# Kernel tuning notes

Measured on AMD Instinct MI355X. Metric: run time of the kernel, lower is better.

Reference implementation:

```python
import jax, jax.numpy as jnp
import numpy as np

IN_DIM = 256
MEM_DIM = 256
DEPTH = 18                    # complete binary tree
N = 2 ** DEPTH - 1            # 262143 nodes; children of i are 2i+1, 2i+2; node 0 is root


def _glorot(k, shape):
    lim = float(np.sqrt(6.0 / (shape[0] + shape[1])))
    return jax.random.uniform(k, shape, jnp.float32, -lim, lim)


def setup_inputs() -> dict:
    key = jax.random.key(0)
    ks = jax.random.split(key, 6)
    inputs = jax.random.normal(ks[0], (N, IN_DIM), jnp.float32)
    Wioux = _glorot(ks[1], (3 * MEM_DIM, IN_DIM))
    bioux = jnp.zeros((3 * MEM_DIM,), jnp.float32)
    Wiouh = _glorot(ks[2], (3 * MEM_DIM, MEM_DIM))
    Wfx = _glorot(ks[3], (MEM_DIM, IN_DIM))
    bfx = jnp.zeros((MEM_DIM,), jnp.float32)
    Wfh = _glorot(ks[4], (MEM_DIM, MEM_DIM))
    fb = jnp.ones((MEM_DIM,), jnp.float32)
    return {"inputs": inputs, "Wioux": Wioux, "bioux": bioux, "Wiouh": Wiouh,
            "Wfx": Wfx, "bfx": bfx, "Wfh": Wfh, "fb": fb}


def reference(inputs, Wioux, bioux, Wiouh, Wfx, bfx, Wfh, fb):
    # Child-Sum TreeLSTM over a complete binary tree, level-wise batched (bottom-up).
    n, _ = inputs.shape
    m = fb.shape[0]
    depth = int(np.log2(n + 1))
    # Input projections for all nodes at once (same math as per-node ioux/fx).
    xiou = inputs @ Wioux.T + bioux          # [N, 3m]
    xf = inputs @ Wfx.T + bfx                # [N, m]
    h_all = jnp.zeros((n, m), inputs.dtype)
    c_all = jnp.zeros((n, m), inputs.dtype)
    for d in range(depth - 1, -1, -1):
        s, e = 2 ** d - 1, 2 ** (d + 1) - 1   # nodes at level d
        if d == depth - 1:
            # Leaves: zero child state -> iouh/fh contribute 0, fc sums to 0.
            i, o, u = jnp.split(xiou[s:e], 3, axis=1)
            i, o, u = jax.nn.sigmoid(i), jax.nn.sigmoid(o), jnp.tanh(u)
            c = i * u
        else:
            node = jnp.arange(s, e)
            ch = jnp.stack([2 * node + 1, 2 * node + 2], axis=1)   # [L, 2]
            ch_h = h_all[ch]                                       # [L, 2, m]
            ch_c = c_all[ch]                                       # [L, 2, m]
            iou = xiou[s:e] + ch_h.sum(axis=1) @ Wiouh.T           # child-sum
            i, o, u = jnp.split(iou, 3, axis=1)
            i, o, u = jax.nn.sigmoid(i), jax.nn.sigmoid(o), jnp.tanh(u)
            f = jax.nn.sigmoid(jnp.einsum('lkm,nm->lkn', ch_h, Wfh)
                               + xf[s:e][:, None, :] + fb)         # per-child forget gate
            c = i * u + (f * ch_c).sum(axis=1)
        h = o * jnp.tanh(c)
        h_all = h_all.at[s:e].set(h)
        c_all = c_all.at[s:e].set(c)
    # (root h, root c, all node hidden states) as in the torch forward
    return h_all[0], c_all[0], h_all
```

## Files before the change

### kernel.cpp

```cpp
#include <hip/hip_runtime.h>


typedef __attribute__((ext_vector_type(8))) short bf16x8;
typedef __attribute__((ext_vector_type(8))) unsigned short us8;
typedef __attribute__((ext_vector_type(4))) float f32x4;
typedef __attribute__((ext_vector_type(4))) float f4;

#define MFMA16(A, B, C) __builtin_amdgcn_mfma_f32_16x16x32_bf16(A, B, C, 0, 0, 0)

__device__ __forceinline__ unsigned short f2b(float f) {
  unsigned int u = __builtin_bit_cast(unsigned int, f);
  u = u + 0x7FFFu + ((u >> 16) & 1u);
  return (unsigned short)(u >> 16);
}
__device__ __forceinline__ float bf2f(unsigned short u) {
  unsigned int v = (unsigned int)u << 16;
  return __builtin_bit_cast(float, v);
}
__device__ __forceinline__ us8 pack8(f4 a, f4 b) {
  us8 r;
  r[0] = f2b(a[0]); r[1] = f2b(a[1]); r[2] = f2b(a[2]); r[3] = f2b(a[3]);
  r[4] = f2b(b[0]); r[5] = f2b(b[1]); r[6] = f2b(b[2]); r[7] = f2b(b[3]);
  return r;
}
__device__ __forceinline__ float sigm(float x) { return 1.0f / (1.0f + __expf(-x)); }
__device__ __forceinline__ float tanh_f(float x) { return 2.0f / (1.0f + __expf(-2.0f * x)) - 1.0f; }

__global__ void pack_w(const float* __restrict__ a,
                       const float* __restrict__ b,
                       const float* __restrict__ c,
                       const float* __restrict__ d,
                       unsigned short* __restrict__ out) {
  int i = blockIdx.x * blockDim.x + threadIdx.x;
  const int A = 768 * 256;
  const int B = A + 768 * 256;
  const int C = B + 256 * 256;
  float v;
  if (i < A)      v = a[i];
  else if (i < B) v = b[i - A];
  else if (i < C) v = c[i - B];
  else            v = d[i - C];
  out[i] = f2b(v);
}

__global__ void conv_x(const float* __restrict__ x, unsigned short* __restrict__ xb, int n8) {
  int i = blockIdx.x * blockDim.x + threadIdx.x;
  if (i >= n8) return;
  f4 a = __builtin_nontemporal_load((const f4*)(x + (size_t)i * 8));
  f4 b = __builtin_nontemporal_load((const f4*)(x + (size_t)i * 8 + 4));
  __builtin_nontemporal_store(pack8(a, b), (us8*)(xb + (size_t)i * 8));
}

template<int LEAF>
__global__ __launch_bounds__(512) __attribute__((amdgpu_waves_per_eu(3, 4)))
void level_k(
    const unsigned short* __restrict__ xb,
    const unsigned short* __restrict__ wb,
    const float* __restrict__ bioux,
    const float* __restrict__ bfx,
    const float* __restrict__ fb,
    float* __restrict__ h_all,
    const unsigned short* __restrict__ hs_r,
    const unsigned short* __restrict__ hbe_r,
    const unsigned int* __restrict__ cp_r,
    unsigned short* __restrict__ hs_w,
    unsigned short* __restrict__ hbe_w,
    unsigned int* __restrict__ cp_w,
    float* __restrict__ out0,
    int s, int L, int T16, int root, int lns)
{
  extern __shared__ unsigned short W[];

  const int tid    = threadIdx.x;
  const int NS     = 1 << lns;
  const int cg     = blockIdx.x >> lns;
  const int stripe = blockIdx.x & (NS - 1);

  const int NP = LEAF ? 3 : 8;
  #pragma unroll 1
  for (int c = tid; c < NP * 512; c += 512) {
    const int p   = c >> 9;
    const int q   = c & 511;
    const int kc  = q >> 6;
    const int kg  = (q >> 4) & 3;
    const int col = q & 15;
    const int po = (p < 3) ? p * 65536
                 : (p < 6) ? 196608 + (p - 3) * 65536
                 : (p == 6) ? 393216 : 458752;
    us8 v = *(const us8*)(wb + po + (size_t)(cg * 16 + col) * 256 + kc * 32 + kg * 8);
    *(us8*)(W + p * 4096 + ((kc * 4 + kg) * 16 + col) * 8) = v;
  }
  __syncthreads();

  const int lane = tid & 63;
  const int wv   = tid >> 6;
  const int lm   = lane & 15;
  const int kgl  = lane >> 4;
  const int colc = cg * 16 + lm;

  const unsigned short* LW = W + kgl * 128 + lm * 8;

  const float bi_ = bioux[colc];
  const float bo_ = bioux[256 + colc];
  const float bu_ = bioux[512 + colc];
  const float bf_ = LEAF ? 0.f : (bfx[colc] + fb[colc]);

  const int Tper = (T16 + NS - 1) >> lns;
  const int t0   = stripe * Tper;
  const int tE   = (t0 + Tper < T16) ? (t0 + Tper) : T16;

  for (int t = t0 + wv; t < tE; t += 8) {
    const int tb16  = t * 16;
    const int drow0 = tb16 + kgl * 4;
    const unsigned short* xr = xb + (size_t)(s + tb16 + lm) * 256 + kgl * 8;
    const f32x4 z4 = {0.f, 0.f, 0.f, 0.f};

    if (!LEAF) {
      const unsigned short* hbr = hbe_r + (size_t)(tb16 + lm) * 256 + kgl * 8;
      const unsigned short* hsr = hs_r  + (size_t)(tb16 + lm) * 256 + kgl * 8;

      unsigned int cpv[4];
      #pragma unroll
      for (int r = 0; r < 4; ++r)
        cpv[r] = cp_r[(size_t)(drow0 + r) * 256 + colc];

      f32x4 xf = z4, f1h = z4, ai = z4, ao = z4, au = z4, fs = z4;
      #pragma unroll 2
      for (int kc = 0; kc < 8; ++kc) {
        bf16x8 ax = *(const bf16x8*)(xr  + kc * 32);
        bf16x8 a1 = *(const bf16x8*)(hbr + kc * 32);
        bf16x8 ah = *(const bf16x8*)(hsr + kc * 32);
        bf16x8 b6 = *(const bf16x8*)(LW + 6 * 4096 + kc * 512);
        bf16x8 b0 = *(const bf16x8*)(LW + 0 * 4096 + kc * 512);
        bf16x8 b1 = *(const bf16x8*)(LW + 1 * 4096 + kc * 512);
        bf16x8 b2 = *(const bf16x8*)(LW + 2 * 4096 + kc * 512);
        bf16x8 b7 = *(const bf16x8*)(LW + 7 * 4096 + kc * 512);
        bf16x8 b3 = *(const bf16x8*)(LW + 3 * 4096 + kc * 512);
        bf16x8 b4 = *(const bf16x8*)(LW + 4 * 4096 + kc * 512);
        bf16x8 b5 = *(const bf16x8*)(LW + 5 * 4096 + kc * 512);
        xf  = MFMA16(ax, b6, xf);
        ai  = MFMA16(ax, b0, ai);
        ao  = MFMA16(ax, b1, ao);
        au  = MFMA16(ax, b2, au);
        f1h = MFMA16(a1, b7, f1h);
        ai  = MFMA16(ah, b3, ai);
        ao  = MFMA16(ah, b4, ao);
        au  = MFMA16(ah, b5, au);
        fs  = MFMA16(ah, b7, fs);
      }

      float hv4[4], cv4[4];
      #pragma unroll
      for (int r = 0; r < 4; ++r) {
        const float i_ = sigm(ai[r] + bi_);
        const float u_ = tanh_f(au[r] + bu_);
        const float o_ = sigm(ao[r] + bo_);
        const float f1 = sigm(xf[r] + f1h[r] + bf_);
        const float f2 = sigm(xf[r] + fs[r] - f1h[r] + bf_);
        const float c1 = bf2f((unsigned short)(cpv[r] & 0xffffu));
        const float c2 = bf2f((unsigned short)(cpv[r] >> 16));
        const float c_ = i_ * u_ + f1 * c1 + f2 * c2;
        const float h_ = o_ * tanh_f(c_);
        cv4[r] = c_; hv4[r] = h_;
        const int j = drow0 + r;
        if (j < L)
          __builtin_nontemporal_store(h_, h_all + (size_t)(s + j) * 256 + colc);
      }
      if (root) {
        if (drow0 == 0) { out0[colc] = hv4[0]; out0[256 + colc] = cv4[0]; }
      } else {
        #pragma unroll
        for (int rp = 0; rp < 2; ++rp) {
          const int j0 = drow0 + rp * 2;
          if (j0 + 1 < L) {
            const int pp = j0 >> 1;
            hs_w [(size_t)pp * 256 + colc] = f2b(hv4[rp*2] + hv4[rp*2+1]);
            hbe_w[(size_t)pp * 256 + colc] = f2b(hv4[rp*2]);
            cp_w [(size_t)pp * 256 + colc] =
                (unsigned int)f2b(cv4[rp*2]) | ((unsigned int)f2b(cv4[rp*2+1]) << 16);
          }
        }
      }
    } else {
      f32x4 ai = z4, ao = z4, au = z4;
      #pragma unroll 4
      for (int kc = 0; kc < 8; ++kc) {
        bf16x8 ax = *(const bf16x8*)(xr + kc * 32);
        bf16x8 b0 = *(const bf16x8*)(LW + 0 * 4096 + kc * 512);
        bf16x8 b1 = *(const bf16x8*)(LW + 1 * 4096 + kc * 512);
        bf16x8 b2 = *(const bf16x8*)(LW + 2 * 4096 + kc * 512);
        ai = MFMA16(ax, b0, ai);
        ao = MFMA16(ax, b1, ao);
        au = MFMA16(ax, b2, au);
      }
      float hv4[4], cv4[4];
      #pragma unroll
      for (int r = 0; r < 4; ++r) {
        const float i_ = sigm(ai[r] + bi_);
        const float u_ = tanh_f(au[r] + bu_);
        const float o_ = sigm(ao[r] + bo_);
        const float c_ = i_ * u_;
        const float h_ = o_ * tanh_f(c_);
        cv4[r] = c_; hv4[r] = h_;
        __builtin_nontemporal_store(h_, h_all + (size_t)(s + drow0 + r) * 256 + colc);
      }
      #pragma unroll
      for (int rp = 0; rp < 2; ++rp) {
        const int pp = (drow0 + rp * 2) >> 1;
        hs_w [(size_t)pp * 256 + colc] = f2b(hv4[rp*2] + hv4[rp*2+1]);
        hbe_w[(size_t)pp * 256 + colc] = f2b(hv4[rp*2]);
        cp_w [(size_t)pp * 256 + colc] =
            (unsigned int)f2b(cv4[rp*2]) | ((unsigned int)f2b(cv4[rp*2+1]) << 16);
      }
    }
  }
}

extern "C" void kernel_launch(void* const* d_in, const int* in_sizes, int n_in,
                              void* d_out, int out_size, void* d_ws, size_t ws_size,
                              hipStream_t stream) {
  const float* inputs = (const float*)d_in[0];
  const float* Wioux  = (const float*)d_in[1];
  const float* bioux  = (const float*)d_in[2];
  const float* Wiouh  = (const float*)d_in[3];
  const float* Wfx    = (const float*)d_in[4];
  const float* bfx    = (const float*)d_in[5];
  const float* Wfh    = (const float*)d_in[6];
  const float* fb     = (const float*)d_in[7];

  const int N = in_sizes[0] / 256;
  int depth = 0;
  while (((1 << depth) - 1) < N) ++depth;

  float* out   = (float*)d_out;
  float* h_all = out + 512;

  static bool attr_done = false;
  if (!attr_done) {
    hipFuncSetAttribute((const void*)level_k<0>,
                        hipFuncAttributeMaxDynamicSharedMemorySize, 8 * 8192);
    hipFuncSetAttribute((const void*)level_k<1>,
                        hipFuncAttributeMaxDynamicSharedMemorySize, 3 * 8192);
    attr_done = true;
  }

  char* p = (char*)d_ws;
  unsigned short* hs0  = (unsigned short*)p; p += (size_t)65536 * 256 * 2;
  unsigned short* hbe0 = (unsigned short*)p; p += (size_t)65536 * 256 * 2;
  unsigned int*   cp0  = (unsigned int*)p;   p += (size_t)65536 * 256 * 4;
  unsigned short* hs1  = (unsigned short*)p; p += (size_t)32768 * 256 * 2;
  unsigned short* hbe1 = (unsigned short*)p; p += (size_t)32768 * 256 * 2;
  unsigned int*   cp1  = (unsigned int*)p;   p += (size_t)32768 * 256 * 4;
  unsigned short* xb   = (unsigned short*)p; p += (size_t)N * 256 * 2;
  unsigned short* wb   = (unsigned short*)p;

  pack_w<<<2048, 256, 0, stream>>>(Wioux, Wiouh, Wfx, Wfh, wb);
  {
    const int n8 = (N * 256) / 8;
    conv_x<<<(n8 + 255) / 256, 256, 0, stream>>>(inputs, xb, n8);
  }

  for (int d = depth - 1; d >= 0; --d) {
    const int L = 1 << d;
    const int s = L - 1;
    const int T16 = (L + 15) / 16;
    int lg = 0; while ((1 << (lg + 1)) <= T16) ++lg;
    int lns = lg - 3; if (lns < 0) lns = 0; if (lns > 5) lns = 5;
    const int rp_ = d & 1, wp_ = (d - 1) & 1;
    const unsigned short* hs_r  = rp_ ? hs1 : hs0;
    const unsigned short* hbe_r = rp_ ? hbe1 : hbe0;
    const unsigned int*   cp_r  = rp_ ? cp1 : cp0;
    unsigned short* hs_w  = wp_ ? hs1 : hs0;
    unsigned short* hbe_w = wp_ ? hbe1 : hbe0;
    unsigned int*   cp_w  = wp_ ? cp1 : cp0;
    if (d == depth - 1) {
      level_k<1><<<16 * 64, 512, 3 * 8192, stream>>>(
          xb, wb, bioux, bfx, fb, h_all,
          hs_r, hbe_r, cp_r, hs_w, hbe_w, cp_w, out, s, L, T16, 0, 6);
    } else {
      level_k<0><<<16 << lns, 512, 8 * 8192, stream>>>(
          xb, wb, bioux, bfx, fb, h_all,
          hs_r, hbe_r, cp_r, hs_w, hbe_w, cp_w, out, s, L, T16, (d == 0) ? 1 : 0, lns);
    }
  }
}
```

Baseline: 803.8 us.

## Store x and child-h buffers in MFMA-tiled layout for contiguous fragment loads

The bf16 input conversion now writes each tree level into a padded, 16-row-tiled layout in which each k-chunk of a 16-row tile is contiguous. The hs/hbe child-state buffers are written in the same tiled layout. The A-operand loads for the MFMAs then read 512-byte contiguous blocks instead of rows strided by 512 bytes, which should improve coalescing. In exchange the scattered 2-byte stores of h partial sums become strided in the tiled layout, and a little padding is added to the workspace.

```diff
diff --git a/kernel.cpp b/kernel.cpp
--- a/kernel.cpp
+++ b/kernel.cpp
@@ -43,18 +43,24 @@
   out[i] = f2b(v);
 }
 
-__global__ void conv_x(const float* __restrict__ x, unsigned short* __restrict__ xb, int n8) {
+__global__ void conv_x(const float* __restrict__ x, unsigned short* __restrict__ xb, int n32) {
   int i = blockIdx.x * blockDim.x + threadIdx.x;
-  if (i >= n8) return;
-  f4 a = __builtin_nontemporal_load((const f4*)(x + (size_t)i * 8));
-  f4 b = __builtin_nontemporal_load((const f4*)(x + (size_t)i * 8 + 4));
-  __builtin_nontemporal_store(pack8(a, b), (us8*)(xb + (size_t)i * 8));
+  if (i >= n32) return;
+  const int n = i >> 5, g = i & 31;
+  f4 a = __builtin_nontemporal_load((const f4*)(x + (size_t)n * 256 + g * 8));
+  f4 b = __builtin_nontemporal_load((const f4*)(x + (size_t)n * 256 + g * 8 + 4));
+  const int d = 31 - __clz(n + 1);
+  const int r = n - ((1 << d) - 1);
+  const size_t base = (size_t)((d < 4) ? d * 16 : 48 + (1 << d)) * 256;
+  const size_t off = base + ((size_t)((r >> 4) * 8 + (g >> 2)) * 16 + (r & 15)) * 32
+                     + (g & 3) * 8;
+  __builtin_nontemporal_store(pack8(a, b), (us8*)(xb + off));
 }
 
 template<int LEAF>
 __global__ __launch_bounds__(512) __attribute__((amdgpu_waves_per_eu(3, 4)))
 void level_k(
-    const unsigned short* __restrict__ xb,
+    const unsigned short* __restrict__ xlv,
     const unsigned short* __restrict__ wb,
     const float* __restrict__ bioux,
     const float* __restrict__ bfx,
@@ -100,6 +106,10 @@
 
   const unsigned short* LW = W + kgl * 128 + lm * 8;
 
+  const int kcw = colc >> 5;
+  const int kgw = (colc >> 3) & 3;
+  const int ew  = colc & 7;
+
   const float bi_ = bioux[colc];
   const float bo_ = bioux[256 + colc];
   const float bu_ = bioux[512 + colc];
@@ -112,12 +122,13 @@
   for (int t = t0 + wv; t < tE; t += 8) {
     const int tb16  = t * 16;
     const int drow0 = tb16 + kgl * 4;
-    const unsigned short* xr = xb + (size_t)(s + tb16 + lm) * 256 + kgl * 8;
+    const size_t abase = (size_t)t * 4096 + lm * 32 + kgl * 8;
+    const unsigned short* xr = xlv + abase;
     const f32x4 z4 = {0.f, 0.f, 0.f, 0.f};
 
     if (!LEAF) {
-      const unsigned short* hbr = hbe_r + (size_t)(tb16 + lm) * 256 + kgl * 8;
-      const unsigned short* hsr = hs_r  + (size_t)(tb16 + lm) * 256 + kgl * 8;
+      const unsigned short* hbr = hbe_r + abase;
+      const unsigned short* hsr = hs_r  + abase;
 
       unsigned int cpv[4];
       #pragma unroll
@@ -127,9 +138,9 @@
       f32x4 xf = z4, f1h = z4, ai = z4, ao = z4, au = z4, fs = z4;
       #pragma unroll 2
       for (int kc = 0; kc < 8; ++kc) {
-        bf16x8 ax = *(const bf16x8*)(xr  + kc * 32);
-        bf16x8 a1 = *(const bf16x8*)(hbr + kc * 32);
-        bf16x8 ah = *(const bf16x8*)(hsr + kc * 32);
+        bf16x8 ax = *(const bf16x8*)(xr  + kc * 512);
+        bf16x8 a1 = *(const bf16x8*)(hbr + kc * 512);
+        bf16x8 ah = *(const bf16x8*)(hsr + kc * 512);
         bf16x8 b6 = *(const bf16x8*)(LW + 6 * 4096 + kc * 512);
         bf16x8 b0 = *(const bf16x8*)(LW + 0 * 4096 + kc * 512);
         bf16x8 b1 = *(const bf16x8*)(LW + 1 * 4096 + kc * 512);
@@ -174,8 +185,10 @@
           const int j0 = drow0 + rp * 2;
           if (j0 + 1 < L) {
             const int pp = j0 >> 1;
-            hs_w [(size_t)pp * 256 + colc] = f2b(hv4[rp*2] + hv4[rp*2+1]);
-            hbe_w[(size_t)pp * 256 + colc] = f2b(hv4[rp*2]);
+            const size_t toff = ((size_t)((pp >> 4) * 8 + kcw) * 16 + (pp & 15)) * 32
+                                + kgw * 8 + ew;
+            hs_w [toff] = f2b(hv4[rp*2] + hv4[rp*2+1]);
+            hbe_w[toff] = f2b(hv4[rp*2]);
             cp_w [(size_t)pp * 256 + colc] =
                 (unsigned int)f2b(cv4[rp*2]) | ((unsigned int)f2b(cv4[rp*2+1]) << 16);
           }
@@ -185,7 +198,7 @@
       f32x4 ai = z4, ao = z4, au = z4;
       #pragma unroll 4
       for (int kc = 0; kc < 8; ++kc) {
-        bf16x8 ax = *(const bf16x8*)(xr + kc * 32);
+        bf16x8 ax = *(const bf16x8*)(xr + kc * 512);
         bf16x8 b0 = *(const bf16x8*)(LW + 0 * 4096 + kc * 512);
         bf16x8 b1 = *(const bf16x8*)(LW + 1 * 4096 + kc * 512);
         bf16x8 b2 = *(const bf16x8*)(LW + 2 * 4096 + kc * 512);
@@ -207,8 +220,10 @@
       #pragma unroll
       for (int rp = 0; rp < 2; ++rp) {
         const int pp = (drow0 + rp * 2) >> 1;
-        hs_w [(size_t)pp * 256 + colc] = f2b(hv4[rp*2] + hv4[rp*2+1]);
-        hbe_w[(size_t)pp * 256 + colc] = f2b(hv4[rp*2]);
+        const size_t toff = ((size_t)((pp >> 4) * 8 + kcw) * 16 + (pp & 15)) * 32
+                            + kgw * 8 + ew;
+        hs_w [toff] = f2b(hv4[rp*2] + hv4[rp*2+1]);
+        hbe_w[toff] = f2b(hv4[rp*2]);
         cp_w [(size_t)pp * 256 + colc] =
             (unsigned int)f2b(cv4[rp*2]) | ((unsigned int)f2b(cv4[rp*2+1]) << 16);
       }
@@ -251,19 +266,20 @@
   unsigned short* hs1  = (unsigned short*)p; p += (size_t)32768 * 256 * 2;
   unsigned short* hbe1 = (unsigned short*)p; p += (size_t)32768 * 256 * 2;
   unsigned int*   cp1  = (unsigned int*)p;   p += (size_t)32768 * 256 * 4;
-  unsigned short* xb   = (unsigned short*)p; p += (size_t)N * 256 * 2;
+  unsigned short* xb   = (unsigned short*)p; p += (size_t)(N + 64) * 256 * 2;
   unsigned short* wb   = (unsigned short*)p;
 
   pack_w<<<2048, 256, 0, stream>>>(Wioux, Wiouh, Wfx, Wfh, wb);
   {
-    const int n8 = (N * 256) / 8;
-    conv_x<<<(n8 + 255) / 256, 256, 0, stream>>>(inputs, xb, n8);
+    const int n32 = N * 32;
+    conv_x<<<(n32 + 255) / 256, 256, 0, stream>>>(inputs, xb, n32);
   }
 
   for (int d = depth - 1; d >= 0; --d) {
     const int L = 1 << d;
     const int s = L - 1;
     const int T16 = (L + 15) / 16;
+    const size_t Pb = (size_t)((d < 4) ? d * 16 : 48 + (1 << d)) * 256;
     int lg = 0; while ((1 << (lg + 1)) <= T16) ++lg;
     int lns = lg - 3; if (lns < 0) lns = 0; if (lns > 5) lns = 5;
     const int rp_ = d & 1, wp_ = (d - 1) & 1;
@@ -275,11 +291,11 @@
     unsigned int*   cp_w  = wp_ ? cp1 : cp0;
     if (d == depth - 1) {
       level_k<1><<<16 * 64, 512, 3 * 8192, stream>>>(
-          xb, wb, bioux, bfx, fb, h_all,
+          xb + Pb, wb, bioux, bfx, fb, h_all,
           hs_r, hbe_r, cp_r, hs_w, hbe_w, cp_w, out, s, L, T16, 0, 6);
     } else {
       level_k<0><<<16 << lns, 512, 8 * 8192, stream>>>(
-          xb, wb, bioux, bfx, fb, h_all,
+          xb + Pb, wb, bioux, bfx, fb, h_all,
           hs_r, hbe_r, cp_r, hs_w, hbe_w, cp_w, out, s, L, T16, (d == 0) ? 1 : 0, lns);
     }
   }
```

Result: faster. 690.3 us (-14.1%).
